# Kernel tuning notes

Measured on AMD Instinct MI355X. Metric: run time of the kernel, lower is better.

## Reference

```python
import jax, jax.numpy as jnp
import numpy as np

SEQ_LEN, BATCH, N_IN, N_OUT, EMB, OUT_LEN = 256, 2048, 64, 64, 128, 128


def _uniform(key, shape, k):
    return jax.random.uniform(key, shape, jnp.float32, -k, k)


def setup_inputs() -> dict:
    key = jax.random.key(0)
    ks = jax.random.split(key, 9)
    kH = 1.0 / np.sqrt(EMB)
    return {
        "x": jax.random.normal(ks[0], (SEQ_LEN, BATCH, N_IN), jnp.float32),
        # encoder LSTM (input_size=N_IN, hidden=EMB), torch gate order i,f,g,o
        "enc_Wih": _uniform(ks[1], (4 * EMB, N_IN), kH),
        "enc_Whh": _uniform(ks[2], (4 * EMB, EMB), kH),
        "enc_b": _uniform(ks[3], (4 * EMB,), kH),
        # decoder LSTM (input_size=N_OUT, hidden=EMB)
        "dec_Wih": _uniform(ks[4], (4 * EMB, N_OUT), kH),
        "dec_Whh": _uniform(ks[5], (4 * EMB, EMB), kH),
        "dec_b": _uniform(ks[6], (4 * EMB,), kH),
        # output Linear EMB -> N_OUT
        "out_W": _uniform(ks[7], (N_OUT, EMB), kH),
        "out_b": _uniform(ks[8], (N_OUT,), kH),
    }


def _lstm_cell(h, c, xt, Wih, Whh, b):
    # torch gate order: i, f, g, o
    gates = xt @ Wih.T + h @ Whh.T + b  # [B, 4H]
    i, f, g, o = jnp.split(gates, 4, axis=-1)
    i, f, o = jax.nn.sigmoid(i), jax.nn.sigmoid(f), jax.nn.sigmoid(o)
    g = jnp.tanh(g)
    c_new = f * c + i * g
    h_new = o * jnp.tanh(c_new)
    return h_new, c_new


def reference(x, enc_Wih, enc_Whh, enc_b, dec_Wih, dec_Whh, dec_b, out_W, out_b):
    B = x.shape[1]
    h0 = jnp.zeros((B, EMB), x.dtype)
    c0 = jnp.zeros((B, EMB), x.dtype)

    # ---- encoder: scan over seq_len ----
    def enc_step(carry, xt):
        h, c = carry
        h, c = _lstm_cell(h, c, xt, enc_Wih, enc_Whh, enc_b)
        return (h, c), None

    (h, c), _ = jax.lax.scan(enc_step, (h0, c0), x)

    x0 = jnp.zeros((B, N_OUT), x.dtype)

    def dec_step(carry, _):
        xt, h, c = carry
        h, c = _lstm_cell(h, c, xt, dec_Wih, dec_Whh, dec_b)
        y = h @ out_W.T + out_b  # [B, N_OUT]
        return (y, h, c), y

    _, ys = jax.lax.scan(dec_step, (x0, h, c), None, length=OUT_LEN)  # [T, B, N_OUT]
    return jnp.transpose(ys, (1, 2, 0))  # [B, N_OUT, T]
```

## Files before the change

kernel.cpp:

```cpp
#include <hip/hip_runtime.h>

#define SEQ    256
#define BATCHN 2048
#define NIN    64
#define H      128
#define NOUT   64
#define TOUT   128
#define BT     16
#define ASTR   200
#define TCH    16

using half8 = _Float16 __attribute__((ext_vector_type(8)));
using f32x4 = float    __attribute__((ext_vector_type(4)));

__device__ __forceinline__ float sigf(float v) {
    return __builtin_amdgcn_rcpf(1.f + __expf(-v));
}
__device__ __forceinline__ float tanhfast(float v) {
    return 1.f - 2.f * __builtin_amdgcn_rcpf(1.f + __expf(2.f * v));
}

__device__ __forceinline__ half8 ldfrag8(const float* __restrict__ p) {
    half8 r;
#pragma unroll
    for (int e = 0; e < 8; ++e) r[e] = (_Float16)p[e];
    return r;
}

__global__ __launch_bounds__(512, 2) void seq2seq_fused(
    const float* __restrict__ x,
    const float* __restrict__ eWih, const float* __restrict__ eWhh, const float* __restrict__ eb,
    const float* __restrict__ dWih, const float* __restrict__ dWhh, const float* __restrict__ db,
    const float* __restrict__ oW,   const float* __restrict__ obv,
    float* __restrict__ out)
{
    __shared__ __align__(16) _Float16 als[2][BT][ASTR];
    __shared__ __align__(16) _Float16 ybuf[TCH][BT][68];

    const int tid  = threadIdx.x;
    const int lane = tid & 63;
    const int w    = tid >> 6;
    const int jl   = lane & 15;
    const int lg   = lane >> 4;
    const int b0   = blockIdx.x * BT;

    half8 wf[4][6];
    float bq[4];
#pragma unroll
    for (int q = 0; q < 4; ++q) {
        const int j = q * H + w * 16 + jl;
#pragma unroll
        for (int kc = 0; kc < 2; ++kc)
            wf[q][kc] = ldfrag8(eWih + j * NIN + kc * 32 + lg * 8);
#pragma unroll
        for (int kc = 2; kc < 6; ++kc)
            wf[q][kc] = ldfrag8(eWhh + j * H + (kc - 2) * 32 + lg * 8);
        bq[q] = eb[j];
    }

    float c[4] = {0.f, 0.f, 0.f, 0.f};

    for (int i = tid; i < 2 * BT * ASTR; i += 512) ((_Float16*)als)[i] = (_Float16)0.f;
    __syncthreads();
    {
        const int xi = tid >> 5, xn = (tid & 31) * 2;
        const float2 xv = *(const float2*)(x + (b0 + xi) * NIN + xn);
        als[0][xi][xn]     = (_Float16)xv.x;
        als[0][xi][xn + 1] = (_Float16)xv.y;
    }
    __syncthreads();

    for (int t = 0; t < SEQ; ++t) {
        const int cur = t & 1, nxt = cur ^ 1;

        const int xi = tid >> 5, xn = (tid & 31) * 2;
        float2 xv = make_float2(0.f, 0.f);
        if (t + 1 < SEQ)
            xv = *(const float2*)(x + ((t + 1) * BATCHN + b0 + xi) * NIN + xn);

        half8 af[6];
#pragma unroll
        for (int kc = 0; kc < 6; ++kc)
            af[kc] = *(const half8*)&als[cur][jl][kc * 32 + lg * 8];

        f32x4 ac[4];
#pragma unroll
        for (int q = 0; q < 4; ++q) {
            f32x4 a = {bq[q], bq[q], bq[q], bq[q]};
#pragma unroll
            for (int kc = 0; kc < 6; ++kc)
                a = __builtin_amdgcn_mfma_f32_16x16x32_f16(af[kc], wf[q][kc], a, 0, 0, 0);
            ac[q] = a;
        }

#pragma unroll
        for (int r = 0; r < 4; ++r) {
            const float ig = sigf(ac[0][r]);
            const float fg = sigf(ac[1][r]);
            const float gg = tanhfast(ac[2][r]);
            const float og = sigf(ac[3][r]);
            c[r] = fg * c[r] + ig * gg;
            const float hv = og * tanhfast(c[r]);
            als[nxt][lg * 4 + r][NIN + w * 16 + jl] = (_Float16)hv;
        }
        als[nxt][xi][xn]     = (_Float16)xv.x;
        als[nxt][xi][xn + 1] = (_Float16)xv.y;
        __syncthreads();
    }

#pragma unroll
    for (int q = 0; q < 4; ++q) {
        const int j = q * H + w * 16 + jl;
#pragma unroll
        for (int kc = 0; kc < 2; ++kc)
            wf[q][kc] = ldfrag8(dWih + j * NIN + kc * 32 + lg * 8);
#pragma unroll
        for (int kc = 2; kc < 6; ++kc)
            wf[q][kc] = ldfrag8(dWhh + j * H + (kc - 2) * 32 + lg * 8);
        bq[q] = db[j];
    }
    half8 of[4];
    float oB = 0.f;
    if (w < 4) {
        const int j = w * 16 + jl;
#pragma unroll
        for (int kc = 0; kc < 4; ++kc)
            of[kc] = ldfrag8(oW + j * H + kc * 32 + lg * 8);
        oB = obv[j];
    }

    for (int s = 0; s < TOUT; ++s) {
        const int cur = s & 1, nxt = cur ^ 1;

        half8 af[6];
#pragma unroll
        for (int kc = 0; kc < 6; ++kc)
            af[kc] = *(const half8*)&als[cur][jl][kc * 32 + lg * 8];

        f32x4 ac[4];
#pragma unroll
        for (int q = 0; q < 4; ++q) {
            f32x4 a = {bq[q], bq[q], bq[q], bq[q]};
#pragma unroll
            for (int kc = 0; kc < 6; ++kc)
                a = __builtin_amdgcn_mfma_f32_16x16x32_f16(af[kc], wf[q][kc], a, 0, 0, 0);
            ac[q] = a;
        }

#pragma unroll
        for (int r = 0; r < 4; ++r) {
            const float ig = sigf(ac[0][r]);
            const float fg = sigf(ac[1][r]);
            const float gg = tanhfast(ac[2][r]);
            const float og = sigf(ac[3][r]);
            c[r] = fg * c[r] + ig * gg;
            const float hv = og * tanhfast(c[r]);
            als[nxt][lg * 4 + r][NIN + w * 16 + jl] = (_Float16)hv;
        }
        __syncthreads();

        if (w < 4) {
            half8 hf[4];
#pragma unroll
            for (int kc = 0; kc < 4; ++kc)
                hf[kc] = *(const half8*)&als[nxt][jl][NIN + kc * 32 + lg * 8];
            f32x4 ya = {oB, oB, oB, oB};
#pragma unroll
            for (int kc = 0; kc < 4; ++kc)
                ya = __builtin_amdgcn_mfma_f32_16x16x32_f16(hf[kc], of[kc], ya, 0, 0, 0);
            const int j = w * 16 + jl;
            const int tt = s & (TCH - 1);
#pragma unroll
            for (int r = 0; r < 4; ++r) {
                const int row = lg * 4 + r;
                const float yv = ya[r];
                als[nxt][row][j] = (_Float16)yv;
                ybuf[tt][row][j] = (_Float16)yv;
            }
        }
        __syncthreads();

        if ((s & (TCH - 1)) == (TCH - 1)) {
            const int t0 = s & ~(TCH - 1);
#pragma unroll
            for (int it = 0; it < 8; ++it) {
                const int slot = it * 512 + tid;
                const int pair = slot >> 2;
                const int tq   = slot & 3;
                const int row  = pair >> 6;
                const int j    = pair & 63;
                float4 v;
                v.x = (float)ybuf[tq * 4 + 0][row][j];
                v.y = (float)ybuf[tq * 4 + 1][row][j];
                v.z = (float)ybuf[tq * 4 + 2][row][j];
                v.w = (float)ybuf[tq * 4 + 3][row][j];
                *(float4*)(out + ((size_t)(b0 + row) * NOUT + j) * TOUT + t0 + tq * 4) = v;
            }
        }
    }
}

extern "C" void kernel_launch(void* const* d_in, const int* in_sizes, int n_in,
                              void* d_out, int out_size, void* d_ws, size_t ws_size,
                              hipStream_t stream) {
    (void)in_sizes; (void)n_in; (void)out_size; (void)d_ws; (void)ws_size;
    const float* x    = (const float*)d_in[0];
    const float* eWih = (const float*)d_in[1];
    const float* eWhh = (const float*)d_in[2];
    const float* eb   = (const float*)d_in[3];
    const float* dWih = (const float*)d_in[4];
    const float* dWhh = (const float*)d_in[5];
    const float* db   = (const float*)d_in[6];
    const float* oW   = (const float*)d_in[7];
    const float* ob   = (const float*)d_in[8];

    seq2seq_fused<<<BATCHN / BT, 512, 0, stream>>>(
        x, eWih, eWhh, eb, dWih, dWhh, db, oW, ob, (float*)d_out);
}
```

Baseline: 397.6 us.

## Halve batch tile to 8 rows and redistribute gate nonlinearities via LDS

Cuts the per-block batch tile from 16 to 8 rows, doubling the grid to 256 blocks so more CUs get work. The MFMA tile stays 16 rows, so half the MFMA rows are padding. Gate pre-activations are staged through a new shared buffer, and each thread then computes the cell update for two (row, hidden) pairs. This spreads the transcendental work across all 512 threads, at the cost of an extra barrier per timestep and LDS round trips.

```diff
diff --git a/kernel.cpp b/kernel.cpp
--- a/kernel.cpp
+++ b/kernel.cpp
@@ -6,7 +6,7 @@
 #define H      128
 #define NOUT   64
 #define TOUT   128
-#define BT     16
+#define BT     8
 #define ASTR   200
 #define TCH    16
 
@@ -25,6 +25,15 @@
 #pragma unroll
     for (int e = 0; e < 8; ++e) r[e] = (_Float16)p[e];
     return r;
+}
+
+__device__ __forceinline__ float lstm_cell(const f32x4 g, float& c) {
+    const float ig = sigf(g[0]);
+    const float fg = sigf(g[1]);
+    const float gg = tanhfast(g[2]);
+    const float og = sigf(g[3]);
+    c = fg * c + ig * gg;
+    return og * tanhfast(c);
 }
 
 __global__ __launch_bounds__(512, 2) void seq2seq_fused(
@@ -34,7 +43,8 @@
     const float* __restrict__ oW,   const float* __restrict__ obv,
     float* __restrict__ out)
 {
-    __shared__ __align__(16) _Float16 als[2][BT][ASTR];
+    __shared__ __align__(16) _Float16 als[2][16][ASTR];
+    __shared__ __align__(16) float    gbuf[BT][H][4];
     __shared__ __align__(16) _Float16 ybuf[TCH][BT][68];
 
     const int tid  = threadIdx.x;
@@ -44,6 +54,11 @@
     const int lg   = lane >> 4;
     const int b0   = blockIdx.x * BT;
 
+    const int er0 = tid >> 7;
+    const int er1 = er0 + 4;
+    const int ec  = tid & 127;
+    float c2[2] = {0.f, 0.f};
+
     half8 wf[4][6];
     float bq[4];
 #pragma unroll
@@ -58,25 +73,21 @@
         bq[q] = eb[j];
     }
 
-    float c[4] = {0.f, 0.f, 0.f, 0.f};
-
-    for (int i = tid; i < 2 * BT * ASTR; i += 512) ((_Float16*)als)[i] = (_Float16)0.f;
+    for (int i = tid; i < 2 * 16 * ASTR; i += 512) ((_Float16*)als)[i] = (_Float16)0.f;
     __syncthreads();
     {
-        const int xi = tid >> 5, xn = (tid & 31) * 2;
-        const float2 xv = *(const float2*)(x + (b0 + xi) * NIN + xn);
-        als[0][xi][xn]     = (_Float16)xv.x;
-        als[0][xi][xn + 1] = (_Float16)xv.y;
+        const int xi = tid >> 6, xn = tid & 63;
+        als[0][xi][xn] = (_Float16)x[(b0 + xi) * NIN + xn];
     }
     __syncthreads();
 
     for (int t = 0; t < SEQ; ++t) {
         const int cur = t & 1, nxt = cur ^ 1;
 
-        const int xi = tid >> 5, xn = (tid & 31) * 2;
-        float2 xv = make_float2(0.f, 0.f);
+        const int xi = tid >> 6, xn = tid & 63;
+        float xv = 0.f;
         if (t + 1 < SEQ)
-            xv = *(const float2*)(x + ((t + 1) * BATCHN + b0 + xi) * NIN + xn);
+            xv = x[((t + 1) * BATCHN + b0 + xi) * NIN + xn];
 
         half8 af[6];
 #pragma unroll
@@ -93,18 +104,24 @@
             ac[q] = a;
         }
 
-#pragma unroll
-        for (int r = 0; r < 4; ++r) {
-            const float ig = sigf(ac[0][r]);
-            const float fg = sigf(ac[1][r]);
-            const float gg = tanhfast(ac[2][r]);
-            const float og = sigf(ac[3][r]);
-            c[r] = fg * c[r] + ig * gg;
-            const float hv = og * tanhfast(c[r]);
-            als[nxt][lg * 4 + r][NIN + w * 16 + jl] = (_Float16)hv;
-        }
-        als[nxt][xi][xn]     = (_Float16)xv.x;
-        als[nxt][xi][xn + 1] = (_Float16)xv.y;
+        if (lg < 2) {
+#pragma unroll
+            for (int r = 0; r < 4; ++r) {
+                f32x4 g = {ac[0][r], ac[1][r], ac[2][r], ac[3][r]};
+                *(f32x4*)&gbuf[lg * 4 + r][w * 16 + jl][0] = g;
+            }
+        }
+        __syncthreads();
+
+        {
+            const f32x4 g0 = *(const f32x4*)&gbuf[er0][ec][0];
+            const f32x4 g1 = *(const f32x4*)&gbuf[er1][ec][0];
+            const float h0 = lstm_cell(g0, c2[0]);
+            const float h1 = lstm_cell(g1, c2[1]);
+            als[nxt][er0][NIN + ec] = (_Float16)h0;
+            als[nxt][er1][NIN + ec] = (_Float16)h1;
+        }
+        als[nxt][xi][xn] = (_Float16)xv;
         __syncthreads();
     }
 
@@ -147,15 +164,22 @@
             ac[q] = a;
         }
 
-#pragma unroll
-        for (int r = 0; r < 4; ++r) {
-            const float ig = sigf(ac[0][r]);
-            const float fg = sigf(ac[1][r]);
-            const float gg = tanhfast(ac[2][r]);
-            const float og = sigf(ac[3][r]);
-            c[r] = fg * c[r] + ig * gg;
-            const float hv = og * tanhfast(c[r]);
-            als[nxt][lg * 4 + r][NIN + w * 16 + jl] = (_Float16)hv;
+        if (lg < 2) {
+#pragma unroll
+            for (int r = 0; r < 4; ++r) {
+                f32x4 g = {ac[0][r], ac[1][r], ac[2][r], ac[3][r]};
+                *(f32x4*)&gbuf[lg * 4 + r][w * 16 + jl][0] = g;
+            }
+        }
+        __syncthreads();
+
+        {
+            const f32x4 g0 = *(const f32x4*)&gbuf[er0][ec][0];
+            const f32x4 g1 = *(const f32x4*)&gbuf[er1][ec][0];
+            const float h0 = lstm_cell(g0, c2[0]);
+            const float h1 = lstm_cell(g1, c2[1]);
+            als[nxt][er0][NIN + ec] = (_Float16)h0;
+            als[nxt][er1][NIN + ec] = (_Float16)h1;
         }
         __syncthreads();
 
@@ -168,14 +192,16 @@
 #pragma unroll
             for (int kc = 0; kc < 4; ++kc)
                 ya = __builtin_amdgcn_mfma_f32_16x16x32_f16(hf[kc], of[kc], ya, 0, 0, 0);
-            const int j = w * 16 + jl;
-            const int tt = s & (TCH - 1);
-#pragma unroll
-            for (int r = 0; r < 4; ++r) {
-                const int row = lg * 4 + r;
-                const float yv = ya[r];
-                als[nxt][row][j] = (_Float16)yv;
-                ybuf[tt][row][j] = (_Float16)yv;
+            if (lg < 2) {
+                const int j = w * 16 + jl;
+                const int tt = s & (TCH - 1);
+#pragma unroll
+                for (int r = 0; r < 4; ++r) {
+                    const int row = lg * 4 + r;
+                    const float yv = ya[r];
+                    als[nxt][row][j] = (_Float16)yv;
+                    ybuf[tt][row][j] = (_Float16)yv;
+                }
             }
         }
         __syncthreads();
@@ -183,7 +209,7 @@
         if ((s & (TCH - 1)) == (TCH - 1)) {
             const int t0 = s & ~(TCH - 1);
 #pragma unroll
-            for (int it = 0; it < 8; ++it) {
+            for (int it = 0; it < 4; ++it) {
                 const int slot = it * 512 + tid;
                 const int pair = slot >> 2;
                 const int tq   = slot & 3;
```

Measured after the change: 412.2 us. +3.7%, slower.

## Fold exp2 scaling into weights, split MFMA chains, batch x prefetch

Applied to the files above, without the earlier changes.

Pre-scales the gate weights and biases by log2(e), or 2*log2(e) for the g gate, so the activations use raw exp2. Sigmoid and tanh are merged so the i*g and o*tanh(c) products each need only one reciprocal. Each gate's six-MFMA dependency chain is split into two independent accumulators to shorten latency. Input loads for four timesteps are issued together per unrolled group, and the step body is shared between encoder and decoder. Launch bounds drop to one block per CU, which frees registers but may lower occupancy, and clamping the exp2 arguments is meant to avoid overflow.

```diff
diff --git a/kernel.cpp b/kernel.cpp
--- a/kernel.cpp
+++ b/kernel.cpp
@@ -9,25 +9,21 @@
 #define BT     16
 #define ASTR   200
 #define TCH    16
+#define LOG2E  1.44269504f
 
 using half8 = _Float16 __attribute__((ext_vector_type(8)));
 using f32x4 = float    __attribute__((ext_vector_type(4)));
 
-__device__ __forceinline__ float sigf(float v) {
-    return __builtin_amdgcn_rcpf(1.f + __expf(-v));
-}
-__device__ __forceinline__ float tanhfast(float v) {
-    return 1.f - 2.f * __builtin_amdgcn_rcpf(1.f + __expf(2.f * v));
-}
-
-__device__ __forceinline__ half8 ldfrag8(const float* __restrict__ p) {
+__device__ __forceinline__ float ex2(float v) { return __builtin_amdgcn_exp2f(v); }
+
+__device__ __forceinline__ half8 ldfrag8(const float* __restrict__ p, float s) {
     half8 r;
 #pragma unroll
-    for (int e = 0; e < 8; ++e) r[e] = (_Float16)p[e];
+    for (int e = 0; e < 8; ++e) r[e] = (_Float16)(p[e] * s);
     return r;
 }
 
-__global__ __launch_bounds__(512, 2) void seq2seq_fused(
+__global__ __launch_bounds__(512, 1) void seq2seq_fused(
     const float* __restrict__ x,
     const float* __restrict__ eWih, const float* __restrict__ eWhh, const float* __restrict__ eb,
     const float* __restrict__ dWih, const float* __restrict__ dWhh, const float* __restrict__ db,
@@ -48,35 +44,31 @@
     float bq[4];
 #pragma unroll
     for (int q = 0; q < 4; ++q) {
+        const float sq = (q == 2) ? 2.f * LOG2E : LOG2E;
         const int j = q * H + w * 16 + jl;
 #pragma unroll
         for (int kc = 0; kc < 2; ++kc)
-            wf[q][kc] = ldfrag8(eWih + j * NIN + kc * 32 + lg * 8);
+            wf[q][kc] = ldfrag8(eWih + j * NIN + kc * 32 + lg * 8, sq);
 #pragma unroll
         for (int kc = 2; kc < 6; ++kc)
-            wf[q][kc] = ldfrag8(eWhh + j * H + (kc - 2) * 32 + lg * 8);
-        bq[q] = eb[j];
+            wf[q][kc] = ldfrag8(eWhh + j * H + (kc - 2) * 32 + lg * 8, sq);
+        bq[q] = eb[j] * sq;
     }
 
     float c[4] = {0.f, 0.f, 0.f, 0.f};
 
     for (int i = tid; i < 2 * BT * ASTR; i += 512) ((_Float16*)als)[i] = (_Float16)0.f;
     __syncthreads();
+    const int xi = tid >> 5, xn = (tid & 31) * 2;
     {
-        const int xi = tid >> 5, xn = (tid & 31) * 2;
         const float2 xv = *(const float2*)(x + (b0 + xi) * NIN + xn);
         als[0][xi][xn]     = (_Float16)xv.x;
         als[0][xi][xn + 1] = (_Float16)xv.y;
     }
     __syncthreads();
 
-    for (int t = 0; t < SEQ; ++t) {
-        const int cur = t & 1, nxt = cur ^ 1;
-
-        const int xi = tid >> 5, xn = (tid & 31) * 2;
-        float2 xv = make_float2(0.f, 0.f);
-        if (t + 1 < SEQ)
-            xv = *(const float2*)(x + ((t + 1) * BATCHN + b0 + xi) * NIN + xn);
+    auto step_body = [&](int cur, float2 xv, bool wx) {
+        const int nxt = cur ^ 1;
 
         half8 af[6];
 #pragma unroll
@@ -86,38 +78,70 @@
         f32x4 ac[4];
 #pragma unroll
         for (int q = 0; q < 4; ++q) {
-            f32x4 a = {bq[q], bq[q], bq[q], bq[q]};
-#pragma unroll
-            for (int kc = 0; kc < 6; ++kc)
-                a = __builtin_amdgcn_mfma_f32_16x16x32_f16(af[kc], wf[q][kc], a, 0, 0, 0);
-            ac[q] = a;
-        }
-
-#pragma unroll
-        for (int r = 0; r < 4; ++r) {
-            const float ig = sigf(ac[0][r]);
-            const float fg = sigf(ac[1][r]);
-            const float gg = tanhfast(ac[2][r]);
-            const float og = sigf(ac[3][r]);
-            c[r] = fg * c[r] + ig * gg;
-            const float hv = og * tanhfast(c[r]);
-            als[nxt][lg * 4 + r][NIN + w * 16 + jl] = (_Float16)hv;
-        }
-        als[nxt][xi][xn]     = (_Float16)xv.x;
-        als[nxt][xi][xn + 1] = (_Float16)xv.y;
+            f32x4 aA = {bq[q], bq[q], bq[q], bq[q]};
+            f32x4 aB = {0.f, 0.f, 0.f, 0.f};
+#pragma unroll
+            for (int kc = 0; kc < 3; ++kc) {
+                aA = __builtin_amdgcn_mfma_f32_16x16x32_f16(af[kc],     wf[q][kc],     aA, 0, 0, 0);
+                aB = __builtin_amdgcn_mfma_f32_16x16x32_f16(af[kc + 3], wf[q][kc + 3], aB, 0, 0, 0);
+            }
+            ac[q] = aA + aB;
+        }
+
+        float A0[4], B0[4], F0[4], D0[4], E2[4], itv[4], hv[4];
+#pragma unroll
+        for (int r = 0; r < 4; ++r) A0[r] = ex2(-ac[0][r]);
+#pragma unroll
+        for (int r = 0; r < 4; ++r) B0[r] = ex2(fminf(ac[2][r], 44.f));
+#pragma unroll
+        for (int r = 0; r < 4; ++r) F0[r] = ex2(-ac[1][r]);
+#pragma unroll
+        for (int r = 0; r < 4; ++r) D0[r] = ex2(-ac[3][r]);
+#pragma unroll
+        for (int r = 0; r < 4; ++r)
+            itv[r] = (B0[r] - 1.f) * __builtin_amdgcn_rcpf((1.f + A0[r]) * (1.f + B0[r]));
+#pragma unroll
+        for (int r = 0; r < 4; ++r)
+            c[r] = __builtin_amdgcn_rcpf(1.f + F0[r]) * c[r] + itv[r];
+#pragma unroll
+        for (int r = 0; r < 4; ++r) E2[r] = ex2(fminf(2.8853901f * c[r], 44.f));
+#pragma unroll
+        for (int r = 0; r < 4; ++r)
+            hv[r] = (E2[r] - 1.f) * __builtin_amdgcn_rcpf((1.f + D0[r]) * (1.f + E2[r]));
+#pragma unroll
+        for (int r = 0; r < 4; ++r)
+            als[nxt][lg * 4 + r][NIN + w * 16 + jl] = (_Float16)hv[r];
+
+        if (wx) {
+            als[nxt][xi][xn]     = (_Float16)xv.x;
+            als[nxt][xi][xn + 1] = (_Float16)xv.y;
+        }
         __syncthreads();
+    };
+
+    for (int tg = 0; tg < SEQ; tg += 4) {
+        float2 xq0 = make_float2(0.f, 0.f), xq1 = xq0, xq2 = xq0, xq3 = xq0;
+        if (tg + 1 < SEQ) xq0 = *(const float2*)(x + ((size_t)(tg + 1) * BATCHN + b0 + xi) * NIN + xn);
+        if (tg + 2 < SEQ) xq1 = *(const float2*)(x + ((size_t)(tg + 2) * BATCHN + b0 + xi) * NIN + xn);
+        if (tg + 3 < SEQ) xq2 = *(const float2*)(x + ((size_t)(tg + 3) * BATCHN + b0 + xi) * NIN + xn);
+        if (tg + 4 < SEQ) xq3 = *(const float2*)(x + ((size_t)(tg + 4) * BATCHN + b0 + xi) * NIN + xn);
+        step_body(0, xq0, true);
+        step_body(1, xq1, true);
+        step_body(0, xq2, true);
+        step_body(1, xq3, true);
     }
 
 #pragma unroll
     for (int q = 0; q < 4; ++q) {
+        const float sq = (q == 2) ? 2.f * LOG2E : LOG2E;
         const int j = q * H + w * 16 + jl;
 #pragma unroll
         for (int kc = 0; kc < 2; ++kc)
-            wf[q][kc] = ldfrag8(dWih + j * NIN + kc * 32 + lg * 8);
+            wf[q][kc] = ldfrag8(dWih + j * NIN + kc * 32 + lg * 8, sq);
 #pragma unroll
         for (int kc = 2; kc < 6; ++kc)
-            wf[q][kc] = ldfrag8(dWhh + j * H + (kc - 2) * 32 + lg * 8);
-        bq[q] = db[j];
+            wf[q][kc] = ldfrag8(dWhh + j * H + (kc - 2) * 32 + lg * 8, sq);
+        bq[q] = db[j] * sq;
     }
     half8 of[4];
     float oB = 0.f;
@@ -125,39 +149,14 @@
         const int j = w * 16 + jl;
 #pragma unroll
         for (int kc = 0; kc < 4; ++kc)
-            of[kc] = ldfrag8(oW + j * H + kc * 32 + lg * 8);
+            of[kc] = ldfrag8(oW + j * H + kc * 32 + lg * 8, 1.f);
         oB = obv[j];
     }
 
     for (int s = 0; s < TOUT; ++s) {
         const int cur = s & 1, nxt = cur ^ 1;
 
-        half8 af[6];
-#pragma unroll
-        for (int kc = 0; kc < 6; ++kc)
-            af[kc] = *(const half8*)&als[cur][jl][kc * 32 + lg * 8];
-
-        f32x4 ac[4];
-#pragma unroll
-        for (int q = 0; q < 4; ++q) {
-            f32x4 a = {bq[q], bq[q], bq[q], bq[q]};
-#pragma unroll
-            for (int kc = 0; kc < 6; ++kc)
-                a = __builtin_amdgcn_mfma_f32_16x16x32_f16(af[kc], wf[q][kc], a, 0, 0, 0);
-            ac[q] = a;
-        }
-
-#pragma unroll
-        for (int r = 0; r < 4; ++r) {
-            const float ig = sigf(ac[0][r]);
-            const float fg = sigf(ac[1][r]);
-            const float gg = tanhfast(ac[2][r]);
-            const float og = sigf(ac[3][r]);
-            c[r] = fg * c[r] + ig * gg;
-            const float hv = og * tanhfast(c[r]);
-            als[nxt][lg * 4 + r][NIN + w * 16 + jl] = (_Float16)hv;
-        }
-        __syncthreads();
+        step_body(cur, make_float2(0.f, 0.f), false);
 
         if (w < 4) {
             half8 hf[4];
```

New measurement: 430.2 us. 8.2% more time.

## Fold output projection into decoder recurrent weights to remove per-step sync

Applied to the files above, without the earlier changes.

Since the decoder input is the previous step's linear output, the change folds dWih·oW into a combined recurrent weight (Whh + Wih·oW) and folds Wih·ob into the bias, so each decoder step needs only the hidden state. The output projection now runs in parallel with the gate MFMAs from the same h fragments, which removes one __syncthreads and the dependent projection from each step's critical path, and cuts the gate K from 192 to 128. The first decoder step with zero input is peeled off, and the fused weights are precomputed per block through shared memory. The fused weights are rounded to fp16 once, which can change numerics slightly.

```diff
diff --git a/kernel.cpp b/kernel.cpp
--- a/kernel.cpp
+++ b/kernel.cpp
@@ -9,6 +9,7 @@
 #define BT     16
 #define ASTR   200
 #define TCH    16
+#define WSTR   136
 
 using half8 = _Float16 __attribute__((ext_vector_type(8)));
 using f32x4 = float    __attribute__((ext_vector_type(4)));
@@ -44,6 +45,8 @@
     const int lg   = lane >> 4;
     const int b0   = blockIdx.x * BT;
 
+    float c[4] = {0.f, 0.f, 0.f, 0.f};
+
     half8 wf[4][6];
     float bq[4];
 #pragma unroll
@@ -58,12 +61,10 @@
         bq[q] = eb[j];
     }
 
-    float c[4] = {0.f, 0.f, 0.f, 0.f};
-
     for (int i = tid; i < 2 * BT * ASTR; i += 512) ((_Float16*)als)[i] = (_Float16)0.f;
     __syncthreads();
+    const int xi = tid >> 5, xn = (tid & 31) * 2;
     {
-        const int xi = tid >> 5, xn = (tid & 31) * 2;
         const float2 xv = *(const float2*)(x + (b0 + xi) * NIN + xn);
         als[0][xi][xn]     = (_Float16)xv.x;
         als[0][xi][xn + 1] = (_Float16)xv.y;
@@ -73,10 +74,9 @@
     for (int t = 0; t < SEQ; ++t) {
         const int cur = t & 1, nxt = cur ^ 1;
 
-        const int xi = tid >> 5, xn = (tid & 31) * 2;
         float2 xv = make_float2(0.f, 0.f);
         if (t + 1 < SEQ)
-            xv = *(const float2*)(x + ((t + 1) * BATCHN + b0 + xi) * NIN + xn);
+            xv = *(const float2*)(x + ((size_t)(t + 1) * BATCHN + b0 + xi) * NIN + xn);
 
         half8 af[6];
 #pragma unroll
@@ -112,41 +112,24 @@
     for (int q = 0; q < 4; ++q) {
         const int j = q * H + w * 16 + jl;
 #pragma unroll
-        for (int kc = 0; kc < 2; ++kc)
-            wf[q][kc] = ldfrag8(dWih + j * NIN + kc * 32 + lg * 8);
-#pragma unroll
-        for (int kc = 2; kc < 6; ++kc)
-            wf[q][kc] = ldfrag8(dWhh + j * H + (kc - 2) * 32 + lg * 8);
+        for (int kc = 0; kc < 4; ++kc)
+            wf[q][kc] = ldfrag8(dWhh + j * H + kc * 32 + lg * 8);
         bq[q] = db[j];
     }
-    half8 of[4];
-    float oB = 0.f;
-    if (w < 4) {
-        const int j = w * 16 + jl;
-#pragma unroll
-        for (int kc = 0; kc < 4; ++kc)
-            of[kc] = ldfrag8(oW + j * H + kc * 32 + lg * 8);
-        oB = obv[j];
-    }
-
-    for (int s = 0; s < TOUT; ++s) {
-        const int cur = s & 1, nxt = cur ^ 1;
-
-        half8 af[6];
-#pragma unroll
-        for (int kc = 0; kc < 6; ++kc)
-            af[kc] = *(const half8*)&als[cur][jl][kc * 32 + lg * 8];
-
+    {
+        half8 af[4];
+#pragma unroll
+        for (int kc = 0; kc < 4; ++kc)
+            af[kc] = *(const half8*)&als[0][jl][NIN + kc * 32 + lg * 8];
         f32x4 ac[4];
 #pragma unroll
         for (int q = 0; q < 4; ++q) {
             f32x4 a = {bq[q], bq[q], bq[q], bq[q]};
 #pragma unroll
-            for (int kc = 0; kc < 6; ++kc)
+            for (int kc = 0; kc < 4; ++kc)
                 a = __builtin_amdgcn_mfma_f32_16x16x32_f16(af[kc], wf[q][kc], a, 0, 0, 0);
             ac[q] = a;
         }
-
 #pragma unroll
         for (int r = 0; r < 4; ++r) {
             const float ig = sigf(ac[0][r]);
@@ -155,33 +138,104 @@
             const float og = sigf(ac[3][r]);
             c[r] = fg * c[r] + ig * gg;
             const float hv = og * tanhfast(c[r]);
-            als[nxt][lg * 4 + r][NIN + w * 16 + jl] = (_Float16)hv;
+            als[1][lg * 4 + r][NIN + w * 16 + jl] = (_Float16)hv;
         }
         __syncthreads();
+    }
+
+    half8 of[4];
+    float oB = 0.f;
+    if (w < 4) {
+        const int j = w * 16 + jl;
+#pragma unroll
+        for (int kc = 0; kc < 4; ++kc)
+            of[kc] = ldfrag8(oW + j * H + kc * 32 + lg * 8);
+        oB = obv[j];
+    }
+
+    {
+        _Float16* mybuf = ((_Float16*)ybuf) + (size_t)w * 16 * WSTR;
+#pragma unroll
+        for (int q = 0; q < 4; ++q) {
+            const int jb = q * H + w * 16;
+            half8 afp[2];
+#pragma unroll
+            for (int k2 = 0; k2 < 2; ++k2)
+                afp[k2] = ldfrag8(dWih + (jb + jl) * NIN + k2 * 32 + lg * 8);
+#pragma unroll 1
+            for (int nt = 0; nt < 8; ++nt) {
+                half8 bf0, bf1;
+#pragma unroll
+                for (int e = 0; e < 8; ++e) {
+                    bf0[e] = (_Float16)oW[(lg * 8 + e) * H + nt * 16 + jl];
+                    bf1[e] = (_Float16)oW[(32 + lg * 8 + e) * H + nt * 16 + jl];
+                }
+                f32x4 acc;
+#pragma unroll
+                for (int r = 0; r < 4; ++r)
+                    acc[r] = dWhh[(jb + lg * 4 + r) * H + nt * 16 + jl];
+                acc = __builtin_amdgcn_mfma_f32_16x16x32_f16(afp[0], bf0, acc, 0, 0, 0);
+                acc = __builtin_amdgcn_mfma_f32_16x16x32_f16(afp[1], bf1, acc, 0, 0, 0);
+#pragma unroll
+                for (int r = 0; r < 4; ++r)
+                    mybuf[(lg * 4 + r) * WSTR + nt * 16 + jl] = (_Float16)acc[r];
+            }
+            __syncthreads();
+#pragma unroll
+            for (int kc = 0; kc < 4; ++kc)
+                wf[q][kc] = *(const half8*)&mybuf[jl * WSTR + kc * 32 + lg * 8];
+            float s = db[jb + jl];
+            for (int m = 0; m < NIN; ++m) s += dWih[(jb + jl) * NIN + m] * obv[m];
+            bq[q] = s;
+            __syncthreads();
+        }
+    }
+
+    for (int i = 1; i <= TOUT; ++i) {
+        const int cur = i & 1, nxt = cur ^ 1;
+
+        half8 af[4];
+#pragma unroll
+        for (int kc = 0; kc < 4; ++kc)
+            af[kc] = *(const half8*)&als[cur][jl][NIN + kc * 32 + lg * 8];
 
         if (w < 4) {
-            half8 hf[4];
+            f32x4 ya = {oB, oB, oB, oB};
 #pragma unroll
             for (int kc = 0; kc < 4; ++kc)
-                hf[kc] = *(const half8*)&als[nxt][jl][NIN + kc * 32 + lg * 8];
-            f32x4 ya = {oB, oB, oB, oB};
-#pragma unroll
-            for (int kc = 0; kc < 4; ++kc)
-                ya = __builtin_amdgcn_mfma_f32_16x16x32_f16(hf[kc], of[kc], ya, 0, 0, 0);
+                ya = __builtin_amdgcn_mfma_f32_16x16x32_f16(af[kc], of[kc], ya, 0, 0, 0);
+            const int tt = (i - 1) & (TCH - 1);
             const int j = w * 16 + jl;
-            const int tt = s & (TCH - 1);
+#pragma unroll
+            for (int r = 0; r < 4; ++r)
+                ybuf[tt][lg * 4 + r][j] = (_Float16)ya[r];
+        }
+
+        if (i < TOUT) {
+            f32x4 ac[4];
+#pragma unroll
+            for (int q = 0; q < 4; ++q) {
+                f32x4 a = {bq[q], bq[q], bq[q], bq[q]};
+#pragma unroll
+                for (int kc = 0; kc < 4; ++kc)
+                    a = __builtin_amdgcn_mfma_f32_16x16x32_f16(af[kc], wf[q][kc], a, 0, 0, 0);
+                ac[q] = a;
+            }
 #pragma unroll
             for (int r = 0; r < 4; ++r) {
-                const int row = lg * 4 + r;
-                const float yv = ya[r];
-                als[nxt][row][j] = (_Float16)yv;
-                ybuf[tt][row][j] = (_Float16)yv;
+                const float ig = sigf(ac[0][r]);
+                const float fg = sigf(ac[1][r]);
+                const float gg = tanhfast(ac[2][r]);
+                const float og = sigf(ac[3][r]);
+                c[r] = fg * c[r] + ig * gg;
+                const float hv = og * tanhfast(c[r]);
+                als[nxt][lg * 4 + r][NIN + w * 16 + jl] = (_Float16)hv;
             }
         }
         __syncthreads();
 
-        if ((s & (TCH - 1)) == (TCH - 1)) {
-            const int t0 = s & ~(TCH - 1);
+        if ((i & (TCH - 1)) == 0) {
+            const int t0 = i - TCH;
 #pragma unroll
             for (int it = 0; it < 8; ++it) {
                 const int slot = it * 512 + tid;
@@ -196,6 +250,7 @@
                 v.w = (float)ybuf[tq * 4 + 3][row][j];
                 *(float4*)(out + ((size_t)(b0 + row) * NOUT + j) * TOUT + t0 + tq * 4) = v;
             }
+            __syncthreads();
         }
     }
 }
```

Measured after the change: 453.3 us. 14.0% more time.
